# Performance work log

Measured on AMD Instinct MI355X. Metric: run time of the kernel, lower is better.

## Reference

```python
import jax, jax.numpy as jnp
import numpy as np

D_MODEL = 1024
NUM_HEADS = 16
HEAD_DIM = D_MODEL // NUM_HEADS
WINDOW = 64
GLOBAL_TOKENS = 4
MAX_SEQ_LEN = 2048
RANDOM_TOKENS = 32
BATCH = 2
SEQ = 2048
NEG = -1.0e9
LN_EPS = 1e-5


def setup_inputs() -> dict:
    key = jax.random.key(0)
    k1, k2, k3, k4 = jax.random.split(key, 4)
    x = jax.random.normal(k1, (BATCH, SEQ, D_MODEL), dtype=jnp.float32)
    w_qkv = jax.random.normal(k2, (D_MODEL, 3 * D_MODEL), dtype=jnp.float32) * (D_MODEL ** -0.5)
    w_out = jax.random.normal(k3, (D_MODEL, D_MODEL), dtype=jnp.float32) * (D_MODEL ** -0.5)
    ln_gamma = jnp.ones((D_MODEL,), dtype=jnp.float32)
    ln_beta = jnp.zeros((D_MODEL,), dtype=jnp.float32)
    rand_idx = jax.random.randint(k4, (MAX_SEQ_LEN, RANDOM_TOKENS), 0, MAX_SEQ_LEN, dtype=jnp.int32)
    return {"x": x, "w_qkv": w_qkv, "w_out": w_out,
            "ln_gamma": ln_gamma, "ln_beta": ln_beta, "rand_idx": rand_idx}


def _build_masks(seq_len, rand_idx):
    i = jnp.arange(seq_len)
    causal = (i[:, None] >= i[None, :]).astype(jnp.float32)  # [L,L], lower-triangular
    # local window mask
    dist = jnp.abs(i[:, None] - i[None, :])
    local = (dist <= WINDOW).astype(jnp.float32) * causal
    # global column mask: columns {0..G-1} u {L-G..L-1}, rows i >= g (== causal on those cols)
    gcols = jnp.concatenate([jnp.arange(GLOBAL_TOKENS), jnp.arange(seq_len - GLOBAL_TOKENS, seq_len)])
    is_gcol = jnp.zeros((seq_len,), jnp.float32).at[gcols].set(1.0)
    glob = is_gcol[None, :] * causal
    # random mask: per-row fixed random columns, then causal-filtered
    ri = rand_idx[:seq_len]  # [L, R]
    rows = jnp.broadcast_to(i[:, None], ri.shape)
    rnd = jnp.zeros((seq_len, seq_len), jnp.float32).at[rows, ri].set(1.0) * causal
    return local, glob, rnd


def reference(x, w_qkv, w_out, ln_gamma, ln_beta, rand_idx):
    B, L, _ = x.shape
    residual = x
    # LayerNorm
    mu = jnp.mean(x, axis=-1, keepdims=True)
    var = jnp.mean(jnp.square(x - mu), axis=-1, keepdims=True)
    xn = (x - mu) * jax.lax.rsqrt(var + LN_EPS) * ln_gamma + ln_beta
    # QKV projection
    qkv = xn @ w_qkv
    q, k, v = jnp.split(qkv, 3, axis=-1)
    q = q.reshape(B, L, NUM_HEADS, HEAD_DIM).transpose(0, 2, 1, 3)  # [B,H,L,D]
    k = k.reshape(B, L, NUM_HEADS, HEAD_DIM).transpose(0, 2, 1, 3)
    v = v.reshape(B, L, NUM_HEADS, HEAD_DIM).transpose(0, 2, 1, 3)
    local, glob, rnd = _build_masks(L, rand_idx)
    raw = jnp.einsum('bhqd,bhkd->bhqk', q, k) / jnp.sqrt(jnp.float32(HEAD_DIM))
    # original sums three masked copies of the same scores:
    # combined = 3*raw + ((1-local)+(1-glob)+(1-rnd)) * NEG
    penalty = (3.0 - (local + glob + rnd)) * NEG  # [L,L]
    combined = 3.0 * raw + penalty[None, None, :, :]
    attn = jax.nn.softmax(combined, axis=-1)
    out = jnp.einsum('bhqk,bhkd->bhqd', attn, v)
    out = out.transpose(0, 2, 1, 3).reshape(B, L, D_MODEL)
    out = out @ w_out
    return out + residual
```

## Files before the change

kernel.cpp:

```cpp
#include <hip/hip_runtime.h>
#include <stdint.h>

typedef __attribute__((ext_vector_type(8))) short shortx8;
typedef __attribute__((ext_vector_type(4))) float floatx4;

static constexpr int SEQ_    = 2048;
static constexpr int DMODEL  = 1024;
static constexpr int HDIM    = 64;
static constexpr int BATCH_  = 2;
static constexpr int NHEADS  = 16;
static constexpr int WINDOW_ = 64;
static constexpr int GTOK    = 4;
static constexpr int RTOK    = 32;
static constexpr int ROWS    = BATCH_ * SEQ_;
static constexpr int QKVN    = 3 * DMODEL;

__device__ inline unsigned short f2bf(float f) {
  union { float f; unsigned int u; } x; x.f = f;
  unsigned int r = (x.u + 0x7FFFu + ((x.u >> 16) & 1u)) >> 16;
  return (unsigned short)r;
}
__device__ inline float bf2f(unsigned short b) {
  union { unsigned int u; float f; } x; x.u = ((unsigned int)b) << 16;
  return x.f;
}

__device__ inline void gload_lds16(const void* g, void* l) {
  __builtin_amdgcn_global_load_lds(
      (const __attribute__((address_space(1))) void*)g,
      (__attribute__((address_space(3))) void*)l, 16, 0, 0);
}

__device__ __forceinline__ void gemm_core_k1024(
    const unsigned short* __restrict__ aSrc0, const unsigned short* __restrict__ aSrc1,
    const unsigned short* __restrict__ bSrc,
    unsigned short* Al, unsigned short* Bl,
    const int wave, const int lane, floatx4 (&acc)[4][2]) {
  const int quad = lane >> 4, l16 = lane & 15;
  const int wm = (wave >> 1) * 64, wn = (wave & 1) * 32;
  unsigned short* AlD0 = Al + (wave * 32) * 32;
  unsigned short* AlD1 = Al + (wave * 32 + 16) * 32;
  unsigned short* BlD  = Bl + (wave * 16) * 32;
  for (int k0 = 0; k0 < 1024; k0 += 32) {
    __syncthreads();
    gload_lds16(aSrc0 + k0, AlD0);
    gload_lds16(aSrc1 + k0, AlD1);
    gload_lds16(bSrc  + k0, BlD);
    __syncthreads();
    shortx8 af[4], bfr[2];
    #pragma unroll
    for (int s = 0; s < 4; s++)
      af[s] = *(const shortx8*)&Al[(wm + s * 16 + l16) * 32 + quad * 8];
    #pragma unroll
    for (int s = 0; s < 2; s++)
      bfr[s] = *(const shortx8*)&Bl[(wn + s * 16 + l16) * 32 + quad * 8];
    #pragma unroll
    for (int sm = 0; sm < 4; sm++)
      #pragma unroll
      for (int sn = 0; sn < 2; sn++)
        acc[sm][sn] = __builtin_amdgcn_mfma_f32_16x16x32_bf16(af[sm], bfr[sn], acc[sm][sn], 0, 0, 0);
  }
}

__global__ __launch_bounds__(256) void k1_prep(
    const float* __restrict__ x, const float* __restrict__ w_qkv,
    const float* __restrict__ w_out, const float* __restrict__ gamma,
    const float* __restrict__ beta, const int* __restrict__ ridx,
    unsigned short* __restrict__ xn, unsigned short* __restrict__ wqT,
    unsigned short* __restrict__ woT, unsigned short* __restrict__ Wvs,
    int* __restrict__ cols, int* __restrict__ cnt, int* __restrict__ tmx,
    int* __restrict__ cnts2, int* __restrict__ qlist) {
  __shared__ float tile[32][33];
  __shared__ float red[4], red2[4];
  __shared__ int rl[RTOK];
  __shared__ int scw, scnw, stm;
  const int bx = blockIdx.x;
  const int t = threadIdx.x;
  if (bx < 3072) {
    int n0 = (bx % 96) * 32, k0 = (bx / 96) * 32;
    int tx = t & 31, ty = t >> 5;
    #pragma unroll
    for (int r = ty; r < 32; r += 8)
      tile[r][tx] = w_qkv[(size_t)(k0 + r) * QKVN + n0 + tx];
    __syncthreads();
    #pragma unroll
    for (int r = ty; r < 32; r += 8)
      wqT[(size_t)(n0 + r) * DMODEL + k0 + tx] = f2bf(tile[tx][r]);
  } else if (bx < 7168) {
    int row = bx - 3072;
    const float4* xr = (const float4*)(x + (size_t)row * DMODEL);
    float4 v = xr[t];
    float s = v.x + v.y + v.z + v.w;
    #pragma unroll
    for (int o = 32; o > 0; o >>= 1) s += __shfl_xor(s, o);
    int wave = t >> 6, lane = t & 63;
    if (lane == 0) red[wave] = s;
    __syncthreads();
    float mean = (red[0] + red[1] + red[2] + red[3]) * (1.0f / DMODEL);
    float dx = v.x - mean, dy = v.y - mean, dz = v.z - mean, dw = v.w - mean;
    float q = dx*dx + dy*dy + dz*dz + dw*dw;
    #pragma unroll
    for (int o = 32; o > 0; o >>= 1) q += __shfl_xor(q, o);
    if (lane == 0) red2[wave] = q;
    __syncthreads();
    float var = (red2[0] + red2[1] + red2[2] + red2[3]) * (1.0f / DMODEL);
    float rs = rsqrtf(var + 1e-5f);
    float4 g = ((const float4*)gamma)[t];
    float4 bb = ((const float4*)beta)[t];
    ushort4 outv;
    outv.x = f2bf(dx * rs * g.x + bb.x);
    outv.y = f2bf(dy * rs * g.y + bb.y);
    outv.z = f2bf(dz * rs * g.z + bb.z);
    outv.w = f2bf(dw * rs * g.w + bb.w);
    ((ushort4*)(xn + (size_t)row * DMODEL))[t] = outv;
  } else if (bx < 8192) {
    int idx = bx - 7168;
    int n0 = (idx & 31) * 32, k0 = (idx >> 5) * 32;
    int tx = t & 31, ty = t >> 5;
    #pragma unroll
    for (int r = ty; r < 32; r += 8)
      tile[r][tx] = w_out[(size_t)(k0 + r) * DMODEL + n0 + tx];
    __syncthreads();
    #pragma unroll
    for (int r = ty; r < 32; r += 8)
      woT[(size_t)(n0 + r) * DMODEL + k0 + tx] = f2bf(tile[tx][r]);
  } else if (bx < 9216) {
    int idx = bx - 8192;
    int v0 = (idx & 31) * 32, k0 = (idx >> 5) * 32;
    int tx = t & 31, ty = t >> 5;
    #pragma unroll
    for (int r = ty; r < 32; r += 8)
      Wvs[(size_t)(k0 + r) * DMODEL + v0 + tx] =
          f2bf(w_qkv[(size_t)(k0 + r) * QKVN + 2 * DMODEL + v0 + tx]);
  } else {
    const int i = bx - 9216;
    if (t < RTOK) rl[t] = ridx[i * RTOK + t];
    if (t == 0) { scw = 0; scnw = 0; stm = 0; }
    __syncthreads();
    const int wstart = (i - WINDOW_ > 0) ? (i - WINDOW_) : 0;
    const int c = t;
    int j = -1;
    bool valid = false;
    bool iswin = (c < 65);
    if (c < 65) {
      j = i - WINDOW_ + c;
      valid = (j >= 0);
    } else if (c < 73) {
      int g = c - 65;
      j = (g < 4) ? g : (SEQ_ - 8 + g);
      valid = (j <= i) && (j < wstart);
    } else if (c < 73 + RTOK) {
      int r = c - 73;
      j = rl[r];
      bool dup = false;
      for (int r2 = 0; r2 < r; r2++) dup = dup || (rl[r2] == j);
      valid = (j <= i) && (j < wstart) && !(j < GTOK || j >= SEQ_ - GTOK) && !dup;
    }
    int tier = -1;
    if (valid) {
      int loc = ((i - j) <= WINDOW_) ? 1 : 0;
      int glb = (j < GTOK || j >= SEQ_ - GTOK) ? 1 : 0;
      int rnd = 0;
      for (int r = 0; r < RTOK; r++) rnd |= (rl[r] == j) ? 1 : 0;
      tier = loc + glb + rnd;
      atomicMax(&stm, tier);
    }
    __syncthreads();
    const int tm = stm;
    if (valid && tier == tm) {
      if (iswin) {
        int pos = atomicAdd(&scw, 1);
        cols[i * 128 + pos] = j;
      } else {
        int pos = 127 - atomicAdd(&scnw, 1);
        cols[i * 128 + pos] = j;
      }
    }
    __syncthreads();
    if (t == 0) {
      cnt[i] = scw + scnw;
      tmx[i] = tm;
      cnts2[i] = scw | (scnw << 16);
      if (i < 68 || i >= SEQ_ - 4) {
        int cc = (i < 68) ? i : 68 + (i - (SEQ_ - 4));
        qlist[cc * 2 + 0] = (tm == 3) ? i : -1;
        qlist[cc * 2 + 1] = (tm == 3) ? (SEQ_ + i) : -1;
      }
    }
  }
}

__global__ __launch_bounds__(256) void k2_wgemm(
    const unsigned short* __restrict__ woT, const unsigned short* __restrict__ Wvs,
    unsigned short* __restrict__ WvoT, const unsigned short* __restrict__ xn,
    const unsigned short* __restrict__ wqT, const int* __restrict__ qlist,
    unsigned short* __restrict__ qf, unsigned short* __restrict__ kf,
    unsigned short* __restrict__ vf) {
  __shared__ unsigned short Al[128 * 32];
  __shared__ unsigned short Bl[64 * 32];
  const int bx = blockIdx.x, t = threadIdx.x;
  const int wave = t >> 6, lane = t & 63;
  const int lrow = lane >> 2, lkoff = (lane & 3) * 8;
  const int quad = lane >> 4, l16 = lane & 15;
  const int wm = (wave >> 1) * 64, wn = (wave & 1) * 32;
  floatx4 acc[4][2] = {};
  if (bx < 128) {
    const int bm = (bx >> 4) * 128, bn = (bx & 15) * 64;
    const unsigned short* a0 = woT + (size_t)(bm + wave * 32 + lrow) * DMODEL + lkoff;
    const unsigned short* a1 = a0 + 16 * DMODEL;
    const unsigned short* b0 = Wvs + (size_t)(bn + wave * 16 + lrow) * DMODEL + lkoff;
    gemm_core_k1024(a0, a1, b0, Al, Bl, wave, lane, acc);
    #pragma unroll
    for (int sm = 0; sm < 4; sm++)
      #pragma unroll
      for (int sn = 0; sn < 2; sn++)
        #pragma unroll
        for (int r = 0; r < 4; r++) {
          int row = bm + wm + sm * 16 + quad * 4 + r;
          int col = bn + wn + sn * 16 + l16;
          WvoT[(size_t)row * DMODEL + col] = f2bf(acc[sm][sn][r]);
        }
  } else {
    const int idx = bx - 128;
    const int job = idx >> 4, bn = (idx & 15) * 64;
    const int wsel = (job < 2) ? 0 : ((job == 2) ? 1 : 2);
    const unsigned short* BT = wqT + (size_t)wsel * DMODEL * DMODEL;
    unsigned short* dstbuf = (job == 0) ? qf
                           : (job == 1) ? (qf + (size_t)128 * DMODEL)
                           : (job == 2) ? kf : vf;
    int rsrc[2];
    #pragma unroll
    for (int q = 0; q < 2; q++) {
      int m = wave * 32 + q * 16 + lrow;
      int row;
      if (job < 2) {
        int s = job * 128 + m;
        int ql = (s < 144) ? qlist[s] : -1;
        row = (ql < 0) ? 0 : ql;
      } else {
        row = (m < 16) ? ((m >> 3) * SEQ_ + (((m & 7) < 4) ? (m & 7) : (SEQ_ - 8 + (m & 7)))) : 0;
      }
      rsrc[q] = row;
    }
    const unsigned short* a0 = xn + (size_t)rsrc[0] * DMODEL + lkoff;
    const unsigned short* a1 = xn + (size_t)rsrc[1] * DMODEL + lkoff;
    const unsigned short* b0 = BT + (size_t)(bn + wave * 16 + lrow) * DMODEL + lkoff;
    gemm_core_k1024(a0, a1, b0, Al, Bl, wave, lane, acc);
    #pragma unroll
    for (int sm = 0; sm < 4; sm++)
      #pragma unroll
      for (int sn = 0; sn < 2; sn++)
        #pragma unroll
        for (int r = 0; r < 4; r++) {
          int m = wm + sm * 16 + quad * 4 + r;
          int col = bn + wn + sn * 16 + l16;
          dstbuf[(size_t)m * DMODEL + col] = f2bf(acc[sm][sn][r]);
        }
  }
}

__global__ __launch_bounds__(256) void k3_xbar(
    const unsigned short* __restrict__ xn, const int* __restrict__ cols,
    const int* __restrict__ cnt, const int* __restrict__ tmx,
    const int* __restrict__ cnts2, const int* __restrict__ qlist,
    const unsigned short* __restrict__ qf, const unsigned short* __restrict__ kf,
    const unsigned short* __restrict__ vf,
    unsigned short* __restrict__ xbar, unsigned short* __restrict__ vbar) {
  const int bx = blockIdx.x, t = threadIdx.x;
  const int wave = t >> 6, lane = t & 63;
  if (bx < 1024) {
    __shared__ unsigned short win[80][256];
    const int b = bx >> 9, rest = bx & 511;
    const int i0 = (rest >> 2) * 16, dimbase = (rest & 3) * 256;
    const size_t xnb = (size_t)(b * SEQ_) * DMODEL;
    const int lo = i0 - 64;
    const int r0 = i0 + wave * 4;
    int tm_[4], cw_[4], cnw_[4], jr0_[4], jr1_[4];
    #pragma unroll
    for (int rr = 0; rr < 4; rr++) {
      const int i = r0 + rr;
      tm_[rr] = tmx[i];
      int c2 = cnts2[i];
      cw_[rr] = c2 & 0xffff; cnw_[rr] = c2 >> 16;
      jr0_[rr] = cols[i * 128 + lane];
      jr1_[rr] = cols[i * 128 + 64 + lane];
    }
    {
      const int l5 = lane & 31, rsub = lane >> 5;
      #pragma unroll 5
      for (int it = 0; it < 10; it++) {
        int r = it * 8 + wave * 2 + rsub;
        int gr = lo + r;
        if (gr >= 0)
          *(int4*)&win[r][l5 * 8] =
              *(const int4*)(xn + xnb + (size_t)gr * DMODEL + dimbase + l5 * 8);
      }
    }
    __syncthreads();
    const unsigned short* xnd = xn + xnb + dimbase + lane * 4;
    auto add4 = [](float4& s, ushort4 v) {
      s.x += bf2f(v.x); s.y += bf2f(v.y); s.z += bf2f(v.z); s.w += bf2f(v.w);
    };
    auto sub4 = [](float4& s, ushort4 v) {
      s.x -= bf2f(v.x); s.y -= bf2f(v.y); s.z -= bf2f(v.z); s.w -= bf2f(v.w);
    };
    float4 ws = {0, 0, 0, 0};
    {
      float4 t1 = {0,0,0,0}, t2 = {0,0,0,0}, t3 = {0,0,0,0};
      const int jstart = (r0 - 64 > 0) ? (r0 - 64) : 0;
      const int cn = r0 - jstart + 1;
      const int base = jstart - lo;
      int c = 0;
      for (; c + 4 <= cn; c += 4) {
        ushort4 v0 = *(const ushort4*)&win[base + c][lane * 4];
        ushort4 v1 = *(const ushort4*)&win[base + c + 1][lane * 4];
        ushort4 v2 = *(const ushort4*)&win[base + c + 2][lane * 4];
        ushort4 v3 = *(const ushort4*)&win[base + c + 3][lane * 4];
        add4(ws, v0); add4(t1, v1); add4(t2, v2); add4(t3, v3);
      }
      for (; c < cn; c++) add4(ws, *(const ushort4*)&win[base + c][lane * 4]);
      ws.x += t1.x + t2.x + t3.x; ws.y += t1.y + t2.y + t3.y;
      ws.z += t1.z + t2.z + t3.z; ws.w += t1.w + t2.w + t3.w;
    }
    for (int rr = 0; rr < 4; rr++) {
      const int i = r0 + rr;
      if (rr > 0) {
        add4(ws, *(const ushort4*)&win[i - lo][lane * 4]);
        int dj = i - 65;
        if (dj >= 0) sub4(ws, *(const ushort4*)&win[dj - lo][lane * 4]);
      }
      const int tm = tm_[rr];
      ushort4 o;
      if (tm == 3) {
        o.x = o.y = o.z = o.w = 0;
      } else {
        const int cw = cw_[rr], cnw = cnw_[rr];
        const int jr1 = jr1_[rr];
        float4 s;
        if (tm == 1) {
          s = ws;
          float4 t1 = {0,0,0,0}, t2 = {0,0,0,0}, t3 = {0,0,0,0};
          const int bb = 64 - cnw;
          int c = 0;
          for (; c + 8 <= cnw; c += 8) {
            ushort4 v0 = *(const ushort4*)(xnd + (size_t)__shfl(jr1, bb + c)     * DMODEL);
            ushort4 v1 = *(const ushort4*)(xnd + (size_t)__shfl(jr1, bb + c + 1) * DMODEL);
            ushort4 v2 = *(const ushort4*)(xnd + (size_t)__shfl(jr1, bb + c + 2) * DMODEL);
            ushort4 v3 = *(const ushort4*)(xnd + (size_t)__shfl(jr1, bb + c + 3) * DMODEL);
            ushort4 v4 = *(const ushort4*)(xnd + (size_t)__shfl(jr1, bb + c + 4) * DMODEL);
            ushort4 v5 = *(const ushort4*)(xnd + (size_t)__shfl(jr1, bb + c + 5) * DMODEL);
            ushort4 v6 = *(const ushort4*)(xnd + (size_t)__shfl(jr1, bb + c + 6) * DMODEL);
            ushort4 v7 = *(const ushort4*)(xnd + (size_t)__shfl(jr1, bb + c + 7) * DMODEL);
            add4(s, v0); add4(t1, v1); add4(t2, v2); add4(t3, v3);
            add4(s, v4); add4(t1, v5); add4(t2, v6); add4(t3, v7);
          }
          if (c + 4 <= cnw) {
            ushort4 v0 = *(const ushort4*)(xnd + (size_t)__shfl(jr1, bb + c)     * DMODEL);
            ushort4 v1 = *(const ushort4*)(xnd + (size_t)__shfl(jr1, bb + c + 1) * DMODEL);
            ushort4 v2 = *(const ushort4*)(xnd + (size_t)__shfl(jr1, bb + c + 2) * DMODEL);
            ushort4 v3 = *(const ushort4*)(xnd + (size_t)__shfl(jr1, bb + c + 3) * DMODEL);
            add4(s, v0); add4(t1, v1); add4(t2, v2); add4(t3, v3);
            c += 4;
          }
          for (; c < cnw; c++)
            add4(s, *(const ushort4*)(xnd + (size_t)__shfl(jr1, bb + c) * DMODEL));
          s.x += t1.x + t2.x + t3.x; s.y += t1.y + t2.y + t3.y;
          s.z += t1.z + t2.z + t3.z; s.w += t1.w + t2.w + t3.w;
        } else {
          const int jr0 = jr0_[rr];
          s.x = s.y = s.z = s.w = 0.f;
          for (int c = 0; c < cw; c++) {
            int j = (c < 64) ? __shfl(jr0, c) : __shfl(jr1, c - 64);
            add4(s, *(const ushort4*)(xnd + (size_t)j * DMODEL));
          }
          const int bb = 64 - cnw;
          for (int c = 0; c < cnw; c++)
            add4(s, *(const ushort4*)(xnd + (size_t)__shfl(jr1, bb + c) * DMODEL));
        }
        const float inv = 1.0f / (float)(cw + cnw);
        o.x = f2bf(s.x * inv); o.y = f2bf(s.y * inv);
        o.z = f2bf(s.z * inv); o.w = f2bf(s.w * inv);
      }
      *(ushort4*)(xbar + (size_t)(b * SEQ_ + i) * DMODEL + dimbase + lane * 4) = o;
    }
  } else {
    const int s = (bx - 1024) * 4 + wave;
    const int dst = (s < 144) ? qlist[s] : -1;
    if (dst < 0) return;
    const int b = dst >> 11, i = dst & (SEQ_ - 1);
    const int n = cnt[i];
    int myk = 0;
    if (lane < n) {
      int kj = cols[i * 128 + lane];
      myk = b * 8 + ((kj < 4) ? kj : (kj - (SEQ_ - 8)));
    }
    for (int h = 0; h < NHEADS; h++) {
      float qd = bf2f(qf[(size_t)s * DMODEL + h * HDIM + lane]);
      float w[8];
      float m = -1e30f;
      for (int c = 0; c < n; c++) {
        int ks = __shfl(myk, c);
        float kd = bf2f(kf[(size_t)ks * DMODEL + h * HDIM + lane]);
        float p = qd * kd;
        #pragma unroll
        for (int o = 32; o > 0; o >>= 1) p += __shfl_xor(p, o);
        p *= 0.375f;
        w[c] = p;
        m = fmaxf(m, p);
      }
      float denom = 0.f, acc = 0.f;
      for (int c = 0; c < n; c++) {
        int ks = __shfl(myk, c);
        float e = __expf(w[c] - m);
        denom += e;
        acc += e * bf2f(vf[(size_t)ks * DMODEL + h * HDIM + lane]);
      }
      vbar[(size_t)s * DMODEL + h * HDIM + lane] = f2bf(acc / denom);
    }
  }
}

__global__ __launch_bounds__(256) void k4_final(
    const unsigned short* __restrict__ xbar, const unsigned short* __restrict__ WvoT,
    const unsigned short* __restrict__ vbar, const unsigned short* __restrict__ woT,
    const int* __restrict__ qlist, const int* __restrict__ tmx,
    const float* __restrict__ x, float* __restrict__ out) {
  __shared__ unsigned short Al[128 * 32];
  __shared__ unsigned short Bl[64 * 32];
  __shared__ int rowinf[128];
  const int bx = blockIdx.x, t = threadIdx.x;
  const int wave = t >> 6, lane = t & 63;
  const int lrow = lane >> 2, lkoff = (lane & 3) * 8;
  const int quad = lane >> 4, l16 = lane & 15;
  const int wm = (wave >> 1) * 64, wn = (wave & 1) * 32;
  floatx4 acc[4][2] = {};
  if (bx < 512) {
    const int bm = (bx >> 4) * 128, bn = (bx & 15) * 64;
    if (t < 128) rowinf[t] = tmx[(bm + t) & (SEQ_ - 1)];
    const unsigned short* a0 = xbar + (size_t)(bm + wave * 32 + lrow) * DMODEL + lkoff;
    const unsigned short* a1 = a0 + 16 * DMODEL;
    const unsigned short* b0 = WvoT + (size_t)(bn + wave * 16 + lrow) * DMODEL + lkoff;
    gemm_core_k1024(a0, a1, b0, Al, Bl, wave, lane, acc);
    #pragma unroll
    for (int sm = 0; sm < 4; sm++)
      #pragma unroll
      for (int sn = 0; sn < 2; sn++)
        #pragma unroll
        for (int r = 0; r < 4; r++) {
          int m = wm + sm * 16 + quad * 4 + r;
          if (rowinf[m] != 3) {
            int col = bn + wn + sn * 16 + l16;
            size_t off = (size_t)(bm + m) * DMODEL + col;
            out[off] = acc[sm][sn][r] + x[off];
          }
        }
  } else {
    const int idx = bx - 512;
    const int bm = (idx >> 4) * 128, bn = (idx & 15) * 64;
    if (t < 128) {
      int s = bm + t;
      rowinf[t] = (s < 144) ? qlist[s] : -1;
    }
    const unsigned short* a0 = vbar + (size_t)(bm + wave * 32 + lrow) * DMODEL + lkoff;
    const unsigned short* a1 = a0 + 16 * DMODEL;
    const unsigned short* b0 = woT + (size_t)(bn + wave * 16 + lrow) * DMODEL + lkoff;
    gemm_core_k1024(a0, a1, b0, Al, Bl, wave, lane, acc);
    #pragma unroll
    for (int sm = 0; sm < 4; sm++)
      #pragma unroll
      for (int sn = 0; sn < 2; sn++)
        #pragma unroll
        for (int r = 0; r < 4; r++) {
          int m = wm + sm * 16 + quad * 4 + r;
          int dst = rowinf[m];
          if (dst >= 0) {
            int col = bn + wn + sn * 16 + l16;
            size_t off = (size_t)dst * DMODEL + col;
            out[off] = acc[sm][sn][r] + x[off];
          }
        }
  }
}

extern "C" void kernel_launch(void* const* d_in, const int* in_sizes, int n_in,
                              void* d_out, int out_size, void* d_ws, size_t ws_size,
                              hipStream_t stream) {
  const float* x     = (const float*)d_in[0];
  const float* w_qkv = (const float*)d_in[1];
  const float* w_out = (const float*)d_in[2];
  const float* gamma = (const float*)d_in[3];
  const float* beta  = (const float*)d_in[4];
  const int*   ridx  = (const int*)d_in[5];
  float* out = (float*)d_out;

  char* ws = (char*)d_ws;
  size_t off = 0;
  auto alloc = [&](size_t bytes) {
    char* p = ws + off;
    off = (off + bytes + 255) & ~(size_t)255;
    return p;
  };
  unsigned short* xn   = (unsigned short*)alloc((size_t)ROWS * DMODEL * 2);
  unsigned short* wqT  = (unsigned short*)alloc((size_t)QKVN * DMODEL * 2);
  unsigned short* woT  = (unsigned short*)alloc((size_t)DMODEL * DMODEL * 2);
  unsigned short* Wvs  = (unsigned short*)alloc((size_t)DMODEL * DMODEL * 2);
  unsigned short* WvoT = (unsigned short*)alloc((size_t)DMODEL * DMODEL * 2);
  unsigned short* xbar = (unsigned short*)alloc((size_t)ROWS * DMODEL * 2);
  unsigned short* qf   = (unsigned short*)alloc((size_t)256 * DMODEL * 2);
  unsigned short* kf   = (unsigned short*)alloc((size_t)128 * DMODEL * 2);
  unsigned short* vf   = (unsigned short*)alloc((size_t)128 * DMODEL * 2);
  unsigned short* vbar = (unsigned short*)alloc((size_t)256 * DMODEL * 2);
  int* cols  = (int*)alloc((size_t)SEQ_ * 128 * 4);
  int* cnt   = (int*)alloc((size_t)SEQ_ * 4);
  int* tmx   = (int*)alloc((size_t)SEQ_ * 4);
  int* cnts2 = (int*)alloc((size_t)SEQ_ * 4);
  int* qlist = (int*)alloc(256 * 4);

  hipLaunchKernelGGL(k1_prep, dim3(11264), dim3(256), 0, stream,
                     x, w_qkv, w_out, gamma, beta, ridx,
                     xn, wqT, woT, Wvs, cols, cnt, tmx, cnts2, qlist);
  hipLaunchKernelGGL(k2_wgemm, dim3(192), dim3(256), 0, stream,
                     woT, Wvs, WvoT, xn, wqT, qlist, qf, kf, vf);
  hipLaunchKernelGGL(k3_xbar, dim3(1060), dim3(256), 0, stream,
                     xn, cols, cnt, tmx, cnts2, qlist, qf, kf, vf, xbar, vbar);
  hipLaunchKernelGGL(k4_final, dim3(544), dim3(256), 0, stream,
                     xbar, WvoT, vbar, woT, qlist, tmx, x, out);
}
```

Baseline: 168.2 us.

## Widen GEMM tiles to 128x128 and co-schedule weight GEMMs with xbar gather

The shared GEMM core now computes 128x128 tiles per block, with 4x4 MFMA accumulators per wave, instead of 128x64. This halves the block count for the weight, QKV-row and final GEMMs and increases operand reuse per LDS load. The weight-product and special-row QKV GEMMs are folded into one launch with the local-window xbar gather, so they run alongside it rather than in a separate kernel. The small global-row attention step is split into its own launch. The trade-offs are more registers per thread, lower occupancy, and fewer blocks in the final GEMM to cover the device.

Measured after the change: 181.9 us. 8.1% more time.

```diff
diff --git a/kernel.cpp b/kernel.cpp
--- a/kernel.cpp
+++ b/kernel.cpp
@@ -31,33 +31,35 @@
       (__attribute__((address_space(3))) void*)l, 16, 0, 0);
 }
 
-__device__ __forceinline__ void gemm_core_k1024(
+__device__ __forceinline__ void gemm_core128(
     const unsigned short* __restrict__ aSrc0, const unsigned short* __restrict__ aSrc1,
-    const unsigned short* __restrict__ bSrc,
+    const unsigned short* __restrict__ bSrc0, const unsigned short* __restrict__ bSrc1,
     unsigned short* Al, unsigned short* Bl,
-    const int wave, const int lane, floatx4 (&acc)[4][2]) {
+    const int wave, const int lane, floatx4 (&acc)[4][4]) {
   const int quad = lane >> 4, l16 = lane & 15;
-  const int wm = (wave >> 1) * 64, wn = (wave & 1) * 32;
+  const int wm = (wave >> 1) * 64, wn = (wave & 1) * 64;
   unsigned short* AlD0 = Al + (wave * 32) * 32;
-  unsigned short* AlD1 = Al + (wave * 32 + 16) * 32;
-  unsigned short* BlD  = Bl + (wave * 16) * 32;
+  unsigned short* AlD1 = AlD0 + 16 * 32;
+  unsigned short* BlD0 = Bl + (wave * 32) * 32;
+  unsigned short* BlD1 = BlD0 + 16 * 32;
   for (int k0 = 0; k0 < 1024; k0 += 32) {
     __syncthreads();
     gload_lds16(aSrc0 + k0, AlD0);
     gload_lds16(aSrc1 + k0, AlD1);
-    gload_lds16(bSrc  + k0, BlD);
-    __syncthreads();
-    shortx8 af[4], bfr[2];
+    gload_lds16(bSrc0 + k0, BlD0);
+    gload_lds16(bSrc1 + k0, BlD1);
+    __syncthreads();
+    shortx8 af[4], bfr[4];
     #pragma unroll
     for (int s = 0; s < 4; s++)
       af[s] = *(const shortx8*)&Al[(wm + s * 16 + l16) * 32 + quad * 8];
     #pragma unroll
-    for (int s = 0; s < 2; s++)
+    for (int s = 0; s < 4; s++)
       bfr[s] = *(const shortx8*)&Bl[(wn + s * 16 + l16) * 32 + quad * 8];
     #pragma unroll
     for (int sm = 0; sm < 4; sm++)
       #pragma unroll
-      for (int sn = 0; sn < 2; sn++)
+      for (int sn = 0; sn < 4; sn++)
         acc[sm][sn] = __builtin_amdgcn_mfma_f32_16x16x32_bf16(af[sm], bfr[sn], acc[sm][sn], 0, 0, 0);
   }
 }
@@ -190,87 +192,83 @@
   }
 }
 
-__global__ __launch_bounds__(256) void k2_wgemm(
+__global__ __launch_bounds__(256) void k2_fused(
+    const unsigned short* __restrict__ xn, const int* __restrict__ cols,
+    const int* __restrict__ tmx, const int* __restrict__ cnts2,
     const unsigned short* __restrict__ woT, const unsigned short* __restrict__ Wvs,
-    unsigned short* __restrict__ WvoT, const unsigned short* __restrict__ xn,
     const unsigned short* __restrict__ wqT, const int* __restrict__ qlist,
-    unsigned short* __restrict__ qf, unsigned short* __restrict__ kf,
-    unsigned short* __restrict__ vf) {
-  __shared__ unsigned short Al[128 * 32];
-  __shared__ unsigned short Bl[64 * 32];
+    unsigned short* __restrict__ WvoT, unsigned short* __restrict__ qf,
+    unsigned short* __restrict__ kf, unsigned short* __restrict__ vf,
+    unsigned short* __restrict__ xbar) {
+  __shared__ __align__(16) unsigned short smem[80 * 256];
   const int bx = blockIdx.x, t = threadIdx.x;
   const int wave = t >> 6, lane = t & 63;
-  const int lrow = lane >> 2, lkoff = (lane & 3) * 8;
-  const int quad = lane >> 4, l16 = lane & 15;
-  const int wm = (wave >> 1) * 64, wn = (wave & 1) * 32;
-  floatx4 acc[4][2] = {};
-  if (bx < 128) {
-    const int bm = (bx >> 4) * 128, bn = (bx & 15) * 64;
-    const unsigned short* a0 = woT + (size_t)(bm + wave * 32 + lrow) * DMODEL + lkoff;
-    const unsigned short* a1 = a0 + 16 * DMODEL;
-    const unsigned short* b0 = Wvs + (size_t)(bn + wave * 16 + lrow) * DMODEL + lkoff;
-    gemm_core_k1024(a0, a1, b0, Al, Bl, wave, lane, acc);
-    #pragma unroll
-    for (int sm = 0; sm < 4; sm++)
-      #pragma unroll
-      for (int sn = 0; sn < 2; sn++)
+  if (bx < 96) {
+    unsigned short* Al = smem;
+    unsigned short* Bl = smem + 128 * 32;
+    const int lrow = lane >> 2, lkoff = (lane & 3) * 8;
+    const int quad = lane >> 4, l16 = lane & 15;
+    const int wm = (wave >> 1) * 64, wn = (wave & 1) * 64;
+    floatx4 acc[4][4] = {};
+    if (bx < 64) {
+      const int bm = (bx >> 3) * 128, bn = (bx & 7) * 128;
+      const unsigned short* a0 = woT + (size_t)(bm + wave * 32 + lrow) * DMODEL + lkoff;
+      const unsigned short* a1 = a0 + 16 * DMODEL;
+      const unsigned short* b0 = Wvs + (size_t)(bn + wave * 32 + lrow) * DMODEL + lkoff;
+      const unsigned short* b1 = b0 + 16 * DMODEL;
+      gemm_core128(a0, a1, b0, b1, Al, Bl, wave, lane, acc);
+      #pragma unroll
+      for (int sm = 0; sm < 4; sm++)
         #pragma unroll
-        for (int r = 0; r < 4; r++) {
-          int row = bm + wm + sm * 16 + quad * 4 + r;
-          int col = bn + wn + sn * 16 + l16;
-          WvoT[(size_t)row * DMODEL + col] = f2bf(acc[sm][sn][r]);
+        for (int sn = 0; sn < 4; sn++)
+          #pragma unroll
+          for (int r = 0; r < 4; r++) {
+            int row = bm + wm + sm * 16 + quad * 4 + r;
+            int col = bn + wn + sn * 16 + l16;
+            WvoT[(size_t)row * DMODEL + col] = f2bf(acc[sm][sn][r]);
+          }
+    } else {
+      const int idx = bx - 64;
+      const int job = idx >> 3, bn = (idx & 7) * 128;
+      const int wsel = (job < 2) ? 0 : ((job == 2) ? 1 : 2);
+      const unsigned short* BT = wqT + (size_t)wsel * DMODEL * DMODEL;
+      unsigned short* dstbuf = (job == 0) ? qf
+                             : (job == 1) ? (qf + (size_t)128 * DMODEL)
+                             : (job == 2) ? kf : vf;
+      int rsrc[2];
+      #pragma unroll
+      for (int q = 0; q < 2; q++) {
+        int m = wave * 32 + q * 16 + lrow;
+        int row;
+        if (job < 2) {
+          int s = job * 128 + m;
+          int ql = (s < 144) ? qlist[s] : -1;
+          row = (ql < 0) ? 0 : ql;
+        } else {
+          row = (m < 16) ? ((m >> 3) * SEQ_ + (((m & 7) < 4) ? (m & 7) : (SEQ_ - 8 + (m & 7)))) : 0;
         }
+        rsrc[q] = row;
+      }
+      const unsigned short* a0 = xn + (size_t)rsrc[0] * DMODEL + lkoff;
+      const unsigned short* a1 = xn + (size_t)rsrc[1] * DMODEL + lkoff;
+      const unsigned short* b0 = BT + (size_t)(bn + wave * 32 + lrow) * DMODEL + lkoff;
+      const unsigned short* b1 = b0 + 16 * DMODEL;
+      gemm_core128(a0, a1, b0, b1, Al, Bl, wave, lane, acc);
+      #pragma unroll
+      for (int sm = 0; sm < 4; sm++)
+        #pragma unroll
+        for (int sn = 0; sn < 4; sn++)
+          #pragma unroll
+          for (int r = 0; r < 4; r++) {
+            int m = wm + sm * 16 + quad * 4 + r;
+            int col = bn + wn + sn * 16 + l16;
+            dstbuf[(size_t)m * DMODEL + col] = f2bf(acc[sm][sn][r]);
+          }
+    }
   } else {
-    const int idx = bx - 128;
-    const int job = idx >> 4, bn = (idx & 15) * 64;
-    const int wsel = (job < 2) ? 0 : ((job == 2) ? 1 : 2);
-    const unsigned short* BT = wqT + (size_t)wsel * DMODEL * DMODEL;
-    unsigned short* dstbuf = (job == 0) ? qf
-                           : (job == 1) ? (qf + (size_t)128 * DMODEL)
-                           : (job == 2) ? kf : vf;
-    int rsrc[2];
-    #pragma unroll
-    for (int q = 0; q < 2; q++) {
-      int m = wave * 32 + q * 16 + lrow;
-      int row;
-      if (job < 2) {
-        int s = job * 128 + m;
-        int ql = (s < 144) ? qlist[s] : -1;
-        row = (ql < 0) ? 0 : ql;
-      } else {
-        row = (m < 16) ? ((m >> 3) * SEQ_ + (((m & 7) < 4) ? (m & 7) : (SEQ_ - 8 + (m & 7)))) : 0;
-      }
-      rsrc[q] = row;
-    }
-    const unsigned short* a0 = xn + (size_t)rsrc[0] * DMODEL + lkoff;
-    const unsigned short* a1 = xn + (size_t)rsrc[1] * DMODEL + lkoff;
-    const unsigned short* b0 = BT + (size_t)(bn + wave * 16 + lrow) * DMODEL + lkoff;
-    gemm_core_k1024(a0, a1, b0, Al, Bl, wave, lane, acc);
-    #pragma unroll
-    for (int sm = 0; sm < 4; sm++)
-      #pragma unroll
-      for (int sn = 0; sn < 2; sn++)
-        #pragma unroll
-        for (int r = 0; r < 4; r++) {
-          int m = wm + sm * 16 + quad * 4 + r;
-          int col = bn + wn + sn * 16 + l16;
-          dstbuf[(size_t)m * DMODEL + col] = f2bf(acc[sm][sn][r]);
-        }
-  }
-}
-
-__global__ __launch_bounds__(256) void k3_xbar(
-    const unsigned short* __restrict__ xn, const int* __restrict__ cols,
-    const int* __restrict__ cnt, const int* __restrict__ tmx,
-    const int* __restrict__ cnts2, const int* __restrict__ qlist,
-    const unsigned short* __restrict__ qf, const unsigned short* __restrict__ kf,
-    const unsigned short* __restrict__ vf,
-    unsigned short* __restrict__ xbar, unsigned short* __restrict__ vbar) {
-  const int bx = blockIdx.x, t = threadIdx.x;
-  const int wave = t >> 6, lane = t & 63;
-  if (bx < 1024) {
-    __shared__ unsigned short win[80][256];
-    const int b = bx >> 9, rest = bx & 511;
+    auto win = reinterpret_cast<unsigned short (*)[256]>(smem);
+    const int xb = bx - 96;
+    const int b = xb >> 9, rest = xb & 511;
     const int i0 = (rest >> 2) * 16, dimbase = (rest & 3) * 256;
     const size_t xnb = (size_t)(b * SEQ_) * DMODEL;
     const int lo = i0 - 64;
@@ -383,40 +381,48 @@
       }
       *(ushort4*)(xbar + (size_t)(b * SEQ_ + i) * DMODEL + dimbase + lane * 4) = o;
     }
-  } else {
-    const int s = (bx - 1024) * 4 + wave;
-    const int dst = (s < 144) ? qlist[s] : -1;
-    if (dst < 0) return;
-    const int b = dst >> 11, i = dst & (SEQ_ - 1);
-    const int n = cnt[i];
-    int myk = 0;
-    if (lane < n) {
-      int kj = cols[i * 128 + lane];
-      myk = b * 8 + ((kj < 4) ? kj : (kj - (SEQ_ - 8)));
-    }
-    for (int h = 0; h < NHEADS; h++) {
-      float qd = bf2f(qf[(size_t)s * DMODEL + h * HDIM + lane]);
-      float w[8];
-      float m = -1e30f;
-      for (int c = 0; c < n; c++) {
-        int ks = __shfl(myk, c);
-        float kd = bf2f(kf[(size_t)ks * DMODEL + h * HDIM + lane]);
-        float p = qd * kd;
-        #pragma unroll
-        for (int o = 32; o > 0; o >>= 1) p += __shfl_xor(p, o);
-        p *= 0.375f;
-        w[c] = p;
-        m = fmaxf(m, p);
-      }
-      float denom = 0.f, acc = 0.f;
-      for (int c = 0; c < n; c++) {
-        int ks = __shfl(myk, c);
-        float e = __expf(w[c] - m);
-        denom += e;
-        acc += e * bf2f(vf[(size_t)ks * DMODEL + h * HDIM + lane]);
-      }
-      vbar[(size_t)s * DMODEL + h * HDIM + lane] = f2bf(acc / denom);
-    }
+  }
+}
+
+__global__ __launch_bounds__(256) void k3_t3(
+    const int* __restrict__ cols, const int* __restrict__ cnt,
+    const int* __restrict__ qlist,
+    const unsigned short* __restrict__ qf, const unsigned short* __restrict__ kf,
+    const unsigned short* __restrict__ vf, unsigned short* __restrict__ vbar) {
+  const int t = threadIdx.x;
+  const int wave = t >> 6, lane = t & 63;
+  const int s = blockIdx.x * 4 + wave;
+  const int dst = (s < 144) ? qlist[s] : -1;
+  if (dst < 0) return;
+  const int b = dst >> 11, i = dst & (SEQ_ - 1);
+  const int n = cnt[i];
+  int myk = 0;
+  if (lane < n) {
+    int kj = cols[i * 128 + lane];
+    myk = b * 8 + ((kj < 4) ? kj : (kj - (SEQ_ - 8)));
+  }
+  for (int h = 0; h < NHEADS; h++) {
+    float qd = bf2f(qf[(size_t)s * DMODEL + h * HDIM + lane]);
+    float w[8];
+    float m = -1e30f;
+    for (int c = 0; c < n; c++) {
+      int ks = __shfl(myk, c);
+      float kd = bf2f(kf[(size_t)ks * DMODEL + h * HDIM + lane]);
+      float p = qd * kd;
+      #pragma unroll
+      for (int o = 32; o > 0; o >>= 1) p += __shfl_xor(p, o);
+      p *= 0.375f;
+      w[c] = p;
+      m = fmaxf(m, p);
+    }
+    float denom = 0.f, acc = 0.f;
+    for (int c = 0; c < n; c++) {
+      int ks = __shfl(myk, c);
+      float e = __expf(w[c] - m);
+      denom += e;
+      acc += e * bf2f(vf[(size_t)ks * DMODEL + h * HDIM + lane]);
+    }
+    vbar[(size_t)s * DMODEL + h * HDIM + lane] = f2bf(acc / denom);
   }
 }
 
@@ -426,25 +432,26 @@
     const int* __restrict__ qlist, const int* __restrict__ tmx,
     const float* __restrict__ x, float* __restrict__ out) {
   __shared__ unsigned short Al[128 * 32];
-  __shared__ unsigned short Bl[64 * 32];
+  __shared__ unsigned short Bl[128 * 32];
   __shared__ int rowinf[128];
   const int bx = blockIdx.x, t = threadIdx.x;
   const int wave = t >> 6, lane = t & 63;
   const int lrow = lane >> 2, lkoff = (lane & 3) * 8;
   const int quad = lane >> 4, l16 = lane & 15;
-  const int wm = (wave >> 1) * 64, wn = (wave & 1) * 32;
-  floatx4 acc[4][2] = {};
-  if (bx < 512) {
-    const int bm = (bx >> 4) * 128, bn = (bx & 15) * 64;
+  const int wm = (wave >> 1) * 64, wn = (wave & 1) * 64;
+  floatx4 acc[4][4] = {};
+  if (bx < 256) {
+    const int bm = (bx >> 3) * 128, bn = (bx & 7) * 128;
     if (t < 128) rowinf[t] = tmx[(bm + t) & (SEQ_ - 1)];
     const unsigned short* a0 = xbar + (size_t)(bm + wave * 32 + lrow) * DMODEL + lkoff;
     const unsigned short* a1 = a0 + 16 * DMODEL;
-    const unsigned short* b0 = WvoT + (size_t)(bn + wave * 16 + lrow) * DMODEL + lkoff;
-    gemm_core_k1024(a0, a1, b0, Al, Bl, wave, lane, acc);
+    const unsigned short* b0 = WvoT + (size_t)(bn + wave * 32 + lrow) * DMODEL + lkoff;
+    const unsigned short* b1 = b0 + 16 * DMODEL;
+    gemm_core128(a0, a1, b0, b1, Al, Bl, wave, lane, acc);
     #pragma unroll
     for (int sm = 0; sm < 4; sm++)
       #pragma unroll
-      for (int sn = 0; sn < 2; sn++)
+      for (int sn = 0; sn < 4; sn++)
         #pragma unroll
         for (int r = 0; r < 4; r++) {
           int m = wm + sm * 16 + quad * 4 + r;
@@ -455,20 +462,21 @@
           }
         }
   } else {
-    const int idx = bx - 512;
-    const int bm = (idx >> 4) * 128, bn = (idx & 15) * 64;
+    const int idx = bx - 256;
+    const int bm = (idx >> 3) * 128, bn = (idx & 7) * 128;
     if (t < 128) {
       int s = bm + t;
       rowinf[t] = (s < 144) ? qlist[s] : -1;
     }
     const unsigned short* a0 = vbar + (size_t)(bm + wave * 32 + lrow) * DMODEL + lkoff;
     const unsigned short* a1 = a0 + 16 * DMODEL;
-    const unsigned short* b0 = woT + (size_t)(bn + wave * 16 + lrow) * DMODEL + lkoff;
-    gemm_core_k1024(a0, a1, b0, Al, Bl, wave, lane, acc);
+    const unsigned short* b0 = woT + (size_t)(bn + wave * 32 + lrow) * DMODEL + lkoff;
+    const unsigned short* b1 = b0 + 16 * DMODEL;
+    gemm_core128(a0, a1, b0, b1, Al, Bl, wave, lane, acc);
     #pragma unroll
     for (int sm = 0; sm < 4; sm++)
       #pragma unroll
-      for (int sn = 0; sn < 2; sn++)
+      for (int sn = 0; sn < 4; sn++)
         #pragma unroll
         for (int r = 0; r < 4; r++) {
           int m = wm + sm * 16 + quad * 4 + r;
@@ -519,10 +527,11 @@
   hipLaunchKernelGGL(k1_prep, dim3(11264), dim3(256), 0, stream,
                      x, w_qkv, w_out, gamma, beta, ridx,
                      xn, wqT, woT, Wvs, cols, cnt, tmx, cnts2, qlist);
-  hipLaunchKernelGGL(k2_wgemm, dim3(192), dim3(256), 0, stream,
-                     woT, Wvs, WvoT, xn, wqT, qlist, qf, kf, vf);
-  hipLaunchKernelGGL(k3_xbar, dim3(1060), dim3(256), 0, stream,
-                     xn, cols, cnt, tmx, cnts2, qlist, qf, kf, vf, xbar, vbar);
-  hipLaunchKernelGGL(k4_final, dim3(544), dim3(256), 0, stream,
+  hipLaunchKernelGGL(k2_fused, dim3(1120), dim3(256), 0, stream,
+                     xn, cols, tmx, cnts2, woT, Wvs, wqT, qlist,
+                     WvoT, qf, kf, vf, xbar);
+  hipLaunchKernelGGL(k3_t3, dim3(36), dim3(256), 0, stream,
+                     cols, cnt, qlist, qf, kf, vf, vbar);
+  hipLaunchKernelGGL(k4_final, dim3(272), dim3(256), 0, stream,
                      xbar, WvoT, vbar, woT, qlist, tmx, x, out);
 }
```

## Double-buffer GEMM core with BK=64 and XOR-swizzled LDS layout

Applied to the files above, without the earlier changes.

Replaces the single-buffered BK=32 GEMM loop with a double-buffered BK=64 loop. The global-to-LDS load of the next K tile is issued while MFMAs run on the current tile, and the barriers per K step are halved. The LDS layout is XOR-swizzled by row to avoid bank conflicts on the 128-byte rows. The cost is about 48KB of LDS per block, which may reduce occupancy.

New measurement: 165.0 us. No clear change (-1.9%).

```diff
diff --git a/kernel.cpp b/kernel.cpp
--- a/kernel.cpp
+++ b/kernel.cpp
@@ -31,35 +31,54 @@
       (__attribute__((address_space(3))) void*)l, 16, 0, 0);
 }
 
-__device__ __forceinline__ void gemm_core_k1024(
-    const unsigned short* __restrict__ aSrc0, const unsigned short* __restrict__ aSrc1,
-    const unsigned short* __restrict__ bSrc,
-    unsigned short* Al, unsigned short* Bl,
-    const int wave, const int lane, floatx4 (&acc)[4][2]) {
+__device__ __forceinline__ void gemm_bk64_128x64(
+    const unsigned short* __restrict__ aP0, const unsigned short* __restrict__ aP1,
+    const unsigned short* __restrict__ aP2, const unsigned short* __restrict__ aP3,
+    const unsigned short* __restrict__ bP0, const unsigned short* __restrict__ bP1,
+    unsigned short* smem, const int wave, const int lane, floatx4 (&acc)[4][2]) {
   const int quad = lane >> 4, l16 = lane & 15;
   const int wm = (wave >> 1) * 64, wn = (wave & 1) * 32;
-  unsigned short* AlD0 = Al + (wave * 32) * 32;
-  unsigned short* AlD1 = Al + (wave * 32 + 16) * 32;
-  unsigned short* BlD  = Bl + (wave * 16) * 32;
-  for (int k0 = 0; k0 < 1024; k0 += 32) {
-    __syncthreads();
-    gload_lds16(aSrc0 + k0, AlD0);
-    gload_lds16(aSrc1 + k0, AlD1);
-    gload_lds16(bSrc  + k0, BlD);
-    __syncthreads();
-    shortx8 af[4], bfr[2];
-    #pragma unroll
-    for (int s = 0; s < 4; s++)
-      af[s] = *(const shortx8*)&Al[(wm + s * 16 + l16) * 32 + quad * 8];
-    #pragma unroll
-    for (int s = 0; s < 2; s++)
-      bfr[s] = *(const shortx8*)&Bl[(wn + s * 16 + l16) * 32 + quad * 8];
-    #pragma unroll
-    for (int sm = 0; sm < 4; sm++)
-      #pragma unroll
-      for (int sn = 0; sn < 2; sn++)
-        acc[sm][sn] = __builtin_amdgcn_mfma_f32_16x16x32_bf16(af[sm], bfr[sn], acc[sm][sn], 0, 0, 0);
+  const int h = l16 & 7;
+  auto STAGE = [&](int c, int k0) {
+    unsigned short* Ad = smem + c * 12288 + wave * 2048;
+    unsigned short* Bd = smem + c * 12288 + 8192 + wave * 1024;
+    gload_lds16(aP0 + k0, Ad);
+    gload_lds16(aP1 + k0, Ad + 512);
+    gload_lds16(aP2 + k0, Ad + 1024);
+    gload_lds16(aP3 + k0, Ad + 1536);
+    gload_lds16(bP0 + k0, Bd);
+    gload_lds16(bP1 + k0, Bd + 512);
+  };
+  auto COMPUTE = [&](int c) {
+    const unsigned short* A = smem + c * 12288;
+    const unsigned short* B = A + 8192;
+    #pragma unroll
+    for (int kk = 0; kk < 2; kk++) {
+      shortx8 af[4], bfr[2];
+      #pragma unroll
+      for (int s = 0; s < 4; s++)
+        af[s] = *(const shortx8*)&A[(wm + s * 16 + l16) * 64 + (((quad + kk * 4) ^ h) * 8)];
+      #pragma unroll
+      for (int s = 0; s < 2; s++)
+        bfr[s] = *(const shortx8*)&B[(wn + s * 16 + l16) * 64 + (((quad + kk * 4) ^ h) * 8)];
+      #pragma unroll
+      for (int sm = 0; sm < 4; sm++)
+        #pragma unroll
+        for (int sn = 0; sn < 2; sn++)
+          acc[sm][sn] = __builtin_amdgcn_mfma_f32_16x16x32_bf16(af[sm], bfr[sn], acc[sm][sn], 0, 0, 0);
+    }
+  };
+  STAGE(0, 0);
+  __syncthreads();
+  int cur = 0;
+  #pragma unroll 1
+  for (int t = 0; t < 15; ++t) {
+    STAGE(cur ^ 1, (t + 1) * 64);
+    COMPUTE(cur);
+    __syncthreads();
+    cur ^= 1;
   }
+  COMPUTE(cur);
 }
 
 __global__ __launch_bounds__(256) void k1_prep(
@@ -196,20 +215,20 @@
     const unsigned short* __restrict__ wqT, const int* __restrict__ qlist,
     unsigned short* __restrict__ qf, unsigned short* __restrict__ kf,
     unsigned short* __restrict__ vf) {
-  __shared__ unsigned short Al[128 * 32];
-  __shared__ unsigned short Bl[64 * 32];
+  __shared__ __align__(16) unsigned short smem[2 * 12288];
   const int bx = blockIdx.x, t = threadIdx.x;
   const int wave = t >> 6, lane = t & 63;
-  const int lrow = lane >> 2, lkoff = (lane & 3) * 8;
   const int quad = lane >> 4, l16 = lane & 15;
   const int wm = (wave >> 1) * 64, wn = (wave & 1) * 32;
+  const int r8 = lane >> 3;
+  const int swo = ((lane & 7) ^ r8) * 8;
   floatx4 acc[4][2] = {};
   if (bx < 128) {
     const int bm = (bx >> 4) * 128, bn = (bx & 15) * 64;
-    const unsigned short* a0 = woT + (size_t)(bm + wave * 32 + lrow) * DMODEL + lkoff;
-    const unsigned short* a1 = a0 + 16 * DMODEL;
-    const unsigned short* b0 = Wvs + (size_t)(bn + wave * 16 + lrow) * DMODEL + lkoff;
-    gemm_core_k1024(a0, a1, b0, Al, Bl, wave, lane, acc);
+    const unsigned short* a0 = woT + (size_t)(bm + wave * 32 + r8) * DMODEL + swo;
+    const unsigned short* b0 = Wvs + (size_t)(bn + wave * 16 + r8) * DMODEL + swo;
+    gemm_bk64_128x64(a0, a0 + 8 * DMODEL, a0 + 16 * DMODEL, a0 + 24 * DMODEL,
+                     b0, b0 + 8 * DMODEL, smem, wave, lane, acc);
     #pragma unroll
     for (int sm = 0; sm < 4; sm++)
       #pragma unroll
@@ -228,10 +247,10 @@
     unsigned short* dstbuf = (job == 0) ? qf
                            : (job == 1) ? (qf + (size_t)128 * DMODEL)
                            : (job == 2) ? kf : vf;
-    int rsrc[2];
-    #pragma unroll
-    for (int q = 0; q < 2; q++) {
-      int m = wave * 32 + q * 16 + lrow;
+    const unsigned short* aPg[4];
+    #pragma unroll
+    for (int g = 0; g < 4; g++) {
+      int m = wave * 32 + g * 8 + r8;
       int row;
       if (job < 2) {
         int s = job * 128 + m;
@@ -240,12 +259,11 @@
       } else {
         row = (m < 16) ? ((m >> 3) * SEQ_ + (((m & 7) < 4) ? (m & 7) : (SEQ_ - 8 + (m & 7)))) : 0;
       }
-      rsrc[q] = row;
-    }
-    const unsigned short* a0 = xn + (size_t)rsrc[0] * DMODEL + lkoff;
-    const unsigned short* a1 = xn + (size_t)rsrc[1] * DMODEL + lkoff;
-    const unsigned short* b0 = BT + (size_t)(bn + wave * 16 + lrow) * DMODEL + lkoff;
-    gemm_core_k1024(a0, a1, b0, Al, Bl, wave, lane, acc);
+      aPg[g] = xn + (size_t)row * DMODEL + swo;
+    }
+    const unsigned short* b0 = BT + (size_t)(bn + wave * 16 + r8) * DMODEL + swo;
+    gemm_bk64_128x64(aPg[0], aPg[1], aPg[2], aPg[3],
+                     b0, b0 + 8 * DMODEL, smem, wave, lane, acc);
     #pragma unroll
     for (int sm = 0; sm < 4; sm++)
       #pragma unroll
@@ -425,22 +443,22 @@
     const unsigned short* __restrict__ vbar, const unsigned short* __restrict__ woT,
     const int* __restrict__ qlist, const int* __restrict__ tmx,
     const float* __restrict__ x, float* __restrict__ out) {
-  __shared__ unsigned short Al[128 * 32];
-  __shared__ unsigned short Bl[64 * 32];
+  __shared__ __align__(16) unsigned short smem[2 * 12288];
   __shared__ int rowinf[128];
   const int bx = blockIdx.x, t = threadIdx.x;
   const int wave = t >> 6, lane = t & 63;
-  const int lrow = lane >> 2, lkoff = (lane & 3) * 8;
   const int quad = lane >> 4, l16 = lane & 15;
   const int wm = (wave >> 1) * 64, wn = (wave & 1) * 32;
+  const int r8 = lane >> 3;
+  const int swo = ((lane & 7) ^ r8) * 8;
   floatx4 acc[4][2] = {};
   if (bx < 512) {
     const int bm = (bx >> 4) * 128, bn = (bx & 15) * 64;
     if (t < 128) rowinf[t] = tmx[(bm + t) & (SEQ_ - 1)];
-    const unsigned short* a0 = xbar + (size_t)(bm + wave * 32 + lrow) * DMODEL + lkoff;
-    const unsigned short* a1 = a0 + 16 * DMODEL;
-    const unsigned short* b0 = WvoT + (size_t)(bn + wave * 16 + lrow) * DMODEL + lkoff;
-    gemm_core_k1024(a0, a1, b0, Al, Bl, wave, lane, acc);
+    const unsigned short* a0 = xbar + (size_t)(bm + wave * 32 + r8) * DMODEL + swo;
+    const unsigned short* b0 = WvoT + (size_t)(bn + wave * 16 + r8) * DMODEL + swo;
+    gemm_bk64_128x64(a0, a0 + 8 * DMODEL, a0 + 16 * DMODEL, a0 + 24 * DMODEL,
+                     b0, b0 + 8 * DMODEL, smem, wave, lane, acc);
     #pragma unroll
     for (int sm = 0; sm < 4; sm++)
       #pragma unroll
@@ -461,10 +479,10 @@
       int s = bm + t;
       rowinf[t] = (s < 144) ? qlist[s] : -1;
     }
-    const unsigned short* a0 = vbar + (size_t)(bm + wave * 32 + lrow) * DMODEL + lkoff;
-    const unsigned short* a1 = a0 + 16 * DMODEL;
-    const unsigned short* b0 = woT + (size_t)(bn + wave * 16 + lrow) * DMODEL + lkoff;
-    gemm_core_k1024(a0, a1, b0, Al, Bl, wave, lane, acc);
+    const unsigned short* a0 = vbar + (size_t)(bm + wave * 32 + r8) * DMODEL + swo;
+    const unsigned short* b0 = woT + (size_t)(bn + wave * 16 + r8) * DMODEL + swo;
+    gemm_bk64_128x64(a0, a0 + 8 * DMODEL, a0 + 16 * DMODEL, a0 + 24 * DMODEL,
+                     b0, b0 + 8 * DMODEL, smem, wave, lane, acc);
     #pragma unroll
     for (int sm = 0; sm < 4; sm++)
       #pragma unroll
```
